# Performance work log

Hardware: AMD Instinct MI355X
Metric: run time of the kernel (lower is better)

Reference implementation:

```python
import jax, jax.numpy as jnp
import numpy as np

IN_DIM, UNITS, OUT_DIM = 128, 256, 8
DENSITY = 0.5  # 1 - sparsity_level
B, T = 256, 512


def _ncp_dims():
    Nm = OUT_DIM
    Nc = max(int(0.4 * (UNITS - Nm)), 1)   # command neurons (AutoNCP rule)
    Ni = UNITS - Nm - Nc                    # inter neurons
    return Ni, Nc, Nm


def _fanout_mask(rng, n_src, n_dst, fanout):
    # each source connects to `fanout` distinct random destinations
    idx = np.argsort(rng.random((n_src, n_dst)), axis=1)[:, :fanout]
    m = np.zeros((n_src, n_dst), dtype=np.int32)
    m[np.arange(n_src)[:, None], idx] = 1
    return m


def setup_inputs() -> dict:
    key = jax.random.key(0)
    rng = np.random.default_rng(22222)
    Ni, Nc, Nm = _ncp_dims()
    s_fan = max(int(Ni * DENSITY), 1)       # sensory fanout
    i_fan = max(int(Nc * DENSITY), 1)       # inter fanout
    m_fanin = max(int(Nc * DENSITY), 1)     # motor fanin
    M_si = _fanout_mask(rng, IN_DIM, Ni, s_fan)      # sensory -> inter
    M_ic = _fanout_mask(rng, Ni, Nc, i_fan)          # inter -> command
    M_cm = _fanout_mask(rng, Nm, Nc, m_fanin).T      # command -> motor (fanin per motor)

    def layer_mask(M_in, hid):
        # WiredCfCCell: concat input sparsity with dense ones for the recurrent block, then transpose
        return np.concatenate([M_in, np.ones((hid, hid), np.int32)], axis=0).T

    masks = [layer_mask(M_si, Ni), layer_mask(M_ic, Nc), layer_mask(M_cm, Nm)]
    dims = [(IN_DIM, Ni), (Ni, Nc), (Nc, Nm)]
    inp = {}
    for l, (fin, hid) in enumerate(dims):
        cat = fin + hid
        scale = 1.0 / np.sqrt(cat)
        for nm in ("w1", "w2", "wa", "wb"):
            inp[f"{nm}_{l}"] = jnp.asarray(rng.normal(0.0, scale, (hid, cat)).astype(np.float32))
        for nm in ("b1", "b2", "ba", "bb"):
            inp[f"{nm}_{l}"] = jnp.zeros((hid,), jnp.float32)
        inp[f"m{l}"] = jnp.asarray(masks[l])  # int32, constant sparsity mask
    k1, k2 = jax.random.split(key)
    inp["x"] = jax.random.normal(k1, (B, T, IN_DIM), jnp.float32)
    inp["dt"] = jax.random.uniform(k2, (1,), jnp.float32, 0.5, 1.5)
    return inp


def _cfc_cell(xh, w1, b1, w2, b2, wa, ba, wb, bb, m, ts):
    # CfCCell, mode='default', no backbone, sparsity mask on ff1/ff2 weights
    mf = m.astype(w1.dtype)
    ff1 = jnp.tanh(xh @ (w1 * mf).T + b1)
    ff2 = jnp.tanh(xh @ (w2 * mf).T + b2)
    t_interp = jax.nn.sigmoid((xh @ wa.T + ba) * ts + (xh @ wb.T + bb))
    return ff1 * (1.0 - t_interp) + t_interp * ff2


def _forward(x, dt, params, masks):
    Ni, Nc, Nm = _ncp_dims()
    ts = dt[0]
    h0 = jnp.zeros((x.shape[0], Ni), x.dtype)
    h1 = jnp.zeros((x.shape[0], Nc), x.dtype)
    h2 = jnp.zeros((x.shape[0], Nm), x.dtype)
    p0, p1, p2 = params

    def step(carry, xt):
        h0, h1, h2 = carry
        nh0 = _cfc_cell(jnp.concatenate([xt, h0], 1), *p0, masks[0], ts)
        nh1 = _cfc_cell(jnp.concatenate([nh0, h1], 1), *p1, masks[1], ts)
        nh2 = _cfc_cell(jnp.concatenate([nh1, h2], 1), *p2, masks[2], ts)
        return (nh0, nh1, nh2), nh2

    (h0, h1, h2), ys = jax.lax.scan(step, (h0, h1, h2), jnp.swapaxes(x, 0, 1))
    y = jnp.tanh(jnp.swapaxes(ys, 0, 1))          # (B, T, OUT_DIM), tanh output saturation
    h_out = jnp.concatenate([h0, h1, h2], axis=1)  # (B, units)
    return y, h_out


def reference(x, dt,
              w1_0, b1_0, w2_0, b2_0, wa_0, ba_0, wb_0, bb_0, m0,
              w1_1, b1_1, w2_1, b2_1, wa_1, ba_1, wb_1, bb_1, m1,
              w1_2, b1_2, w2_2, b2_2, wa_2, ba_2, wb_2, bb_2, m2):
    params = ((w1_0, b1_0, w2_0, b2_0, wa_0, ba_0, wb_0, bb_0),
              (w1_1, b1_1, w2_1, b2_1, wa_1, ba_1, wb_1, bb_1),
              (w1_2, b1_2, w2_2, b2_2, wa_2, ba_2, wb_2, bb_2))
    return _forward(x, dt, params, (m0, m1, m2))
```

## Files before the change

### kernel.cpp

```cpp
#include <hip/hip_runtime.h>
#include <cmath>


typedef _Float16 f16;
typedef f16 h4 __attribute__((ext_vector_type(4)));
typedef f16 h8 __attribute__((ext_vector_type(8)));
typedef float f4 __attribute__((ext_vector_type(4)));

#define MFMA(a, b, c) __builtin_amdgcn_mfma_f32_16x16x32_f16(a, b, c, 0, 0, 0)
#define RAW_BAR() asm volatile("s_waitcnt lgkmcnt(0)\n\ts_barrier" ::: "memory")

constexpr int IN_DIM = 128, Ni = 149, Nc = 99, Nm = 8;
constexpr int CAT0 = 277, CAT1 = 248, CAT2 = 107;
constexpr int Bsz = 256, Tsz = 512;
constexpr int TC = 128, NCH = 4, NBT = 16;
constexpr int NT0 = 30, NT1 = 21;
constexpr int S0 = 168, S2 = 136;
constexpr size_t XU0_HALVES = (size_t)TC * NBT * NT0 * 256;
constexpr size_t NH0_HALVES = (size_t)TC * NBT * 16 * 160;
constexpr size_t XU1_HALVES = (size_t)TC * NBT * NT1 * 256;
constexpr size_t H0S_HALVES = (size_t)NBT * 16 * S0;
constexpr size_t H12S_HALVES = (size_t)NBT * 2 * 16 * S2;
constexpr size_t YOFF = (size_t)Bsz * Tsz * 8;

constexpr int OFF_X0 = 0;
constexpr int OFF_R0 = 7680;
constexpr int OFF_X1 = 17280;
constexpr int OFF_R12A = 24000;
constexpr int OFF_R12B = 29376;
constexpr int NFRAG = 30144;

__device__ inline float rcpf_(float x) { return __builtin_amdgcn_rcpf(x); }
__device__ __forceinline__ float cfc_h(float a0, float a1, float a2) {
  float e0 = __expf(a0), e1 = __expf(a1), e2 = __expf(a2);
  float pa = 1.f + e0, ma = 1.f - e0;
  float pb = 1.f + e1, mb = 1.f - e1;
  float pc = 1.f + e2;
  float num = fmaf(ma * pb, e2, mb * pa);
  return num * rcpf_(pa * pb * pc);
}
__device__ __forceinline__ float tanhp_(float x) {
  float e = __expf(-2.f * x);
  return (1.f - e) * rcpf_(1.f + e);
}

__global__ __launch_bounds__(256) void pack_kernel(
    const float* __restrict__ w1_0, const float* __restrict__ w2_0,
    const float* __restrict__ wa_0, const float* __restrict__ wb_0,
    const int* __restrict__ m0,
    const float* __restrict__ w1_1, const float* __restrict__ w2_1,
    const float* __restrict__ wa_1, const float* __restrict__ wb_1,
    const int* __restrict__ m1,
    const float* __restrict__ w1_2, const float* __restrict__ w2_2,
    const float* __restrict__ wa_2, const float* __restrict__ wb_2,
    const int* __restrict__ m2, const float* __restrict__ dtp,
    f16* __restrict__ PK) {
  int idx = blockIdx.x * 256 + threadIdx.x;
  if (idx >= NFRAG) return;
  int lane = idx & 63, col = lane & 15, q = lane >> 4;
  float ts = dtp[0];
  const float* Wa = nullptr;
  const float* Wb = nullptr;
  const int* M = nullptr;
  int ld, n, nmax, k0, kmax;
  int mat;
  if (idx < OFF_R0) {
    int p = idx >> 6;
    mat = p / 40; int nt = (p >> 2) % 10, kt = p & 3;
    ld = CAT0; n = nt * 16 + col; nmax = Ni; k0 = kt * 32 + q * 8; kmax = IN_DIM;
    if (mat == 0) { Wa = w1_0; M = m0; }
    else if (mat == 1) { Wa = w2_0; M = m0; }
    else { Wa = wa_0; Wb = wb_0; }
  } else if (idx < OFF_X1) {
    int p = (idx - OFF_R0) >> 6;
    int g = p / 15; mat = (p / 5) % 3; int kt = p % 5;
    ld = CAT0; n = g * 16 + col; nmax = Ni; k0 = IN_DIM + kt * 32 + q * 8; kmax = CAT0;
    if (mat == 0) Wa = w1_0;
    else if (mat == 1) Wa = w2_0;
    else { Wa = wa_0; Wb = wb_0; }
  } else if (idx < OFF_R12A) {
    int p = (idx - OFF_X1) >> 6;
    mat = p / 35; int nt = (p / 5) % 7, kt = p % 5;
    ld = CAT1; n = nt * 16 + col; nmax = Nc; k0 = kt * 32 + q * 8; kmax = Ni;
    if (mat == 0) { Wa = w1_1; M = m1; }
    else if (mat == 1) { Wa = w2_1; M = m1; }
    else { Wa = wa_1; Wb = wb_1; }
  } else if (idx < OFF_R12B) {
    int p = (idx - OFF_R12A) >> 6;
    int wv = p / 12; mat = (p / 4) % 3; int kt = p & 3;
    ld = CAT1; n = wv * 16 + col; nmax = Nc; k0 = Ni + kt * 32 + q * 8; kmax = CAT1;
    if (mat == 0) Wa = w1_1;
    else if (mat == 1) Wa = w2_1;
    else { Wa = wa_1; Wb = wb_1; }
  } else {
    int p = (idx - OFF_R12B) >> 6;
    mat = p / 4; int kt = p & 3;
    ld = CAT2; n = col; nmax = Nm; k0 = kt * 32 + q * 8; kmax = CAT2;
    if (mat == 0) { Wa = w1_2; M = m2; }
    else if (mat == 1) { Wa = w2_2; M = m2; }
    else { Wa = wa_2; Wb = wb_2; }
  }
  h8 r;
#pragma unroll
  for (int j = 0; j < 8; j++) {
    int k = k0 + j;
    float v = 0.f;
    if (n < nmax && k < kmax) {
      if (mat < 2) {
        v = Wa[(size_t)n * ld + k];
        if (M) v *= (float)M[(size_t)n * ld + k];
        v *= -2.f;
      } else {
        v = -(ts * Wa[(size_t)n * ld + k] + Wb[(size_t)n * ld + k]);
      }
    }
    r[j] = (f16)v;
  }
  ((h8*)PK)[idx] = r;
}

__global__ __launch_bounds__(192, 2) void X_kernel(
    const h8* __restrict__ pk, const float* __restrict__ x,
    const f16* __restrict__ NH0, f16* __restrict__ XU0, f16* __restrict__ XU1,
    const float* __restrict__ b1_0, const float* __restrict__ b2_0,
    const float* __restrict__ ba_0, const float* __restrict__ bb_0,
    const float* __restrict__ b1_1, const float* __restrict__ b2_1,
    const float* __restrict__ ba_1, const float* __restrict__ bb_1,
    const float* __restrict__ dtp, int c) {
  __shared__ f16 stg[16 * 136];
  int tid = threadIdx.x;
  int w = tid >> 6, lane = tid & 63, col = lane & 15, q = lane >> 4;
  int wg = blockIdx.x;
  float ts = dtp[0];
  if (wg < 512) {
    if (c < 0) return;
    h8 Bf[7][5];
    float bias[7];
#pragma unroll
    for (int nt = 0; nt < 7; nt++) {
#pragma unroll
      for (int kt = 0; kt < 5; kt++)
        Bf[nt][kt] = pk[OFF_X1 + ((w * 7 + nt) * 5 + kt) * 64 + lane];
      int n = nt * 16 + col;
      bias[nt] = (n < Nc) ? (w == 0 ? -2.f * b1_1[n]
                                    : (w == 1 ? -2.f * b2_1[n]
                                              : -(ts * ba_1[n] + bb_1[n])))
                          : 0.f;
    }
    for (int i = 0; i < 4; i++) {
      int mt = wg * 4 + i;
      const f16* Ab = NH0 + (size_t)mt * 2560;
      h8 A[5];
#pragma unroll
      for (int kt = 0; kt < 5; kt++)
        A[kt] = *(const h8*)(Ab + col * 160 + kt * 32 + q * 8);
#pragma unroll
      for (int nt = 0; nt < 7; nt++) {
        float b = bias[nt];
        f4 acc = {b, b, b, b};
#pragma unroll
        for (int kt = 0; kt < 5; kt++) acc = MFMA(A[kt], Bf[nt][kt], acc);
        h4 o;
#pragma unroll
        for (int rr = 0; rr < 4; rr++) o[rr] = (f16)acc[rr];
        *(h4*)(XU1 + ((size_t)mt * NT1 + w * 7 + nt) * 256 + lane * 4) = o;
      }
    }
  } else {
    int cn = c + 1;
    if (cn >= NCH) return;
    int bx = wg - 512;
    h8 Bf[10][4];
    float bias[10];
#pragma unroll
    for (int nt = 0; nt < 10; nt++) {
#pragma unroll
      for (int kt = 0; kt < 4; kt++)
        Bf[nt][kt] = pk[OFF_X0 + ((w * 10 + nt) * 4 + kt) * 64 + lane];
      int n = nt * 16 + col;
      bias[nt] = (n < Ni) ? (w == 0 ? -2.f * b1_0[n]
                                    : (w == 1 ? -2.f * b2_0[n]
                                              : -(ts * ba_0[n] + bb_0[n])))
                          : 0.f;
    }
    for (int i = 0; i < 4; i++) {
      int mt = bx * 4 + i;
      int tl = mt >> 4, bt = mt & 15;
      int tg = cn * TC + tl;
      if (tid < 128) {
        int sr = tid >> 3, sc = (tid & 7) * 16;
        const float* xp = x + ((size_t)(bt * 16 + sr) * Tsz + tg) * IN_DIM + sc;
        h8 hv0, hv1;
#pragma unroll
        for (int j = 0; j < 8; j++) hv0[j] = (f16)xp[j];
#pragma unroll
        for (int j = 0; j < 8; j++) hv1[j] = (f16)xp[8 + j];
        *(h8*)(stg + sr * 136 + sc) = hv0;
        *(h8*)(stg + sr * 136 + sc + 8) = hv1;
      }
      __syncthreads();
      h8 A[4];
#pragma unroll
      for (int kt = 0; kt < 4; kt++)
        A[kt] = *(const h8*)(stg + col * 136 + kt * 32 + q * 8);
#pragma unroll
      for (int nt = 0; nt < 10; nt++) {
        float b = bias[nt];
        f4 acc = {b, b, b, b};
#pragma unroll
        for (int kt = 0; kt < 4; kt++) acc = MFMA(A[kt], Bf[nt][kt], acc);
        h4 o;
#pragma unroll
        for (int rr = 0; rr < 4; rr++) o[rr] = (f16)acc[rr];
        *(h4*)(XU0 + ((size_t)mt * NT0 + w * 10 + nt) * 256 + lane * 4) = o;
      }
      __syncthreads();
    }
  }
}

__device__ __forceinline__ void r0_step(
    const f16* br, f16* bw, const f16* __restrict__ XU0, f16* __restrict__ NH0,
    float* __restrict__ out, const h8 (&Bf)[3][5], h4 (&xu)[3],
    int t, int tload, int bt, int g, int lane, int col, int q, int n, bool last) {
  h8 A[5];
#pragma unroll
  for (int kt = 0; kt < 5; kt++)
    A[kt] = *(const h8*)(br + col * S0 + kt * 32 + q * 8);
  f4 acc0 = {(float)xu[0][0], (float)xu[0][1], (float)xu[0][2], (float)xu[0][3]};
  f4 acc1 = {(float)xu[1][0], (float)xu[1][1], (float)xu[1][2], (float)xu[1][3]};
  f4 acc2 = {(float)xu[2][0], (float)xu[2][1], (float)xu[2][2], (float)xu[2][3]};
  size_t mtl = (size_t)tload * NBT + bt;
#pragma unroll
  for (int mat = 0; mat < 3; mat++)
    xu[mat] = *(const h4*)(XU0 + (mtl * NT0 + mat * 10 + g) * 256 + lane * 4);
#pragma unroll
  for (int kt = 0; kt < 5; kt++) {
    acc0 = MFMA(A[kt], Bf[0][kt], acc0);
    acc1 = MFMA(A[kt], Bf[1][kt], acc1);
    acc2 = MFMA(A[kt], Bf[2][kt], acc2);
  }
  int mt = t * NBT + bt;
  f16* nh = NH0 + (size_t)mt * 2560;
#pragma unroll
  for (int r = 0; r < 4; r++) {
    int m = q * 4 + r;
    float h = cfc_h(acc0[r], acc1[r], acc2[r]);
    f16 h16 = (f16)h;
    bw[m * S0 + n] = h16;
    nh[m * 160 + n] = h16;
    if (last && n < Ni) out[YOFF + (size_t)(bt * 16 + m) * 256 + n] = h;
  }
}

__device__ __forceinline__ void r12l1_step(
    const f16* br, f16* bw, const f16* __restrict__ XU1, float* __restrict__ out,
    const h8 (&Bf)[3][4], h4 (&xu)[3],
    int tload, int bt, int w, int lane, int col, int q, int n, bool last) {
  h8 A[4];
#pragma unroll
  for (int kt = 0; kt < 4; kt++)
    A[kt] = *(const h8*)(br + col * S2 + kt * 32 + q * 8);
  f4 acc0 = {(float)xu[0][0], (float)xu[0][1], (float)xu[0][2], (float)xu[0][3]};
  f4 acc1 = {(float)xu[1][0], (float)xu[1][1], (float)xu[1][2], (float)xu[1][3]};
  f4 acc2 = {(float)xu[2][0], (float)xu[2][1], (float)xu[2][2], (float)xu[2][3]};
  size_t mtl = (size_t)tload * NBT + bt;
#pragma unroll
  for (int mat = 0; mat < 3; mat++)
    xu[mat] = *(const h4*)(XU1 + (mtl * NT1 + mat * 7 + w) * 256 + lane * 4);
#pragma unroll
  for (int kt = 0; kt < 4; kt++) {
    acc0 = MFMA(A[kt], Bf[0][kt], acc0);
    acc1 = MFMA(A[kt], Bf[1][kt], acc1);
    acc2 = MFMA(A[kt], Bf[2][kt], acc2);
  }
#pragma unroll
  for (int r = 0; r < 4; r++) {
    int m = q * 4 + r;
    float h = cfc_h(acc0[r], acc1[r], acc2[r]);
    if (n < Nc) {
      bw[m * S2 + n] = (f16)h;
      if (last) out[YOFF + (size_t)(bt * 16 + m) * 256 + Ni + n] = h;
    }
  }
}

__device__ __forceinline__ void r12l2_step(
    const f16* rb, f16* wb, float* __restrict__ out, const h8 (&Bf)[3][4],
    float bn0, float bn1, float bn2, int tg, int bt, int col, int q, bool last) {
  h8 A[4];
#pragma unroll
  for (int kt = 0; kt < 4; kt++)
    A[kt] = *(const h8*)(rb + col * S2 + kt * 32 + q * 8);
  f4 acc0 = {bn0, bn0, bn0, bn0};
  f4 acc1 = {bn1, bn1, bn1, bn1};
  f4 acc2 = {bn2, bn2, bn2, bn2};
#pragma unroll
  for (int kt = 0; kt < 4; kt++) {
    acc0 = MFMA(A[kt], Bf[0][kt], acc0);
    acc1 = MFMA(A[kt], Bf[1][kt], acc1);
    acc2 = MFMA(A[kt], Bf[2][kt], acc2);
  }
#pragma unroll
  for (int r = 0; r < 4; r++) {
    int m = q * 4 + r;
    float h = cfc_h(acc0[r], acc1[r], acc2[r]);
    if (col < Nm) {
      out[((size_t)(bt * 16 + m) * Tsz + tg) * 8 + col] = tanhp_(h);
      wb[m * S2 + Nc + col] = (f16)h;
      if (last) out[YOFF + (size_t)(bt * 16 + m) * 256 + Ni + Nc + col] = h;
    }
  }
}

__global__ __launch_bounds__(640) void R_kernel(
    const h8* __restrict__ pk,
    const float* __restrict__ c1, const float* __restrict__ c2,
    const float* __restrict__ ca, const float* __restrict__ cb,
    const float* __restrict__ dtp, const f16* __restrict__ XU0,
    const f16* __restrict__ XU1, f16* __restrict__ NH0,
    f16* __restrict__ H0S, f16* __restrict__ H12S, float* __restrict__ out, int c) {
  __shared__ __align__(16) char smem[2 * 16 * S0 * 2];
  int tid = threadIdx.x;
  int g = tid >> 6, lane = tid & 63, col = lane & 15, q = lane >> 4;
  int wg = blockIdx.x;

  if (wg < NBT) {
    if (c >= NCH) return;
    f16(*buf)[16 * S0] = (f16(*)[16 * S0])smem;
    int bt = wg;
    int n = g * 16 + col;
    h8 Bf[3][5];
#pragma unroll
    for (int mat = 0; mat < 3; mat++)
#pragma unroll
      for (int kt = 0; kt < 5; kt++)
        Bf[mat][kt] = pk[OFF_R0 + ((g * 3 + mat) * 5 + kt) * 64 + lane];

    for (int idx = tid; idx < 16 * S0; idx += 640) {
      buf[0][idx] = (c == 0) ? (f16)0.f : H0S[(size_t)bt * 16 * S0 + idx];
      buf[1][idx] = (f16)0.f;
    }
    __syncthreads();

    h4 xuA[3], xuB[3];
#pragma unroll
    for (int mat = 0; mat < 3; mat++) {
      xuA[mat] = *(const h4*)(XU0 + ((size_t)bt * NT0 + mat * 10 + g) * 256 + lane * 4);
      xuB[mat] =
          *(const h4*)(XU0 + ((size_t)(NBT + bt) * NT0 + mat * 10 + g) * 256 + lane * 4);
    }

    for (int t = 0; t < TC; t += 2) {
      bool lastA = (c == NCH - 1) && (t == TC - 1);
      int tlA = (t + 2 < TC) ? t + 2 : t;
      r0_step(buf[0], buf[1], XU0, NH0, out, Bf, xuA, t, tlA, bt, g, lane, col, q, n,
              lastA);
      RAW_BAR();
      bool lastB = (c == NCH - 1) && (t + 1 == TC - 1);
      int tlB = (t + 3 < TC) ? t + 3 : t + 1;
      r0_step(buf[1], buf[0], XU0, NH0, out, Bf, xuB, t + 1, tlB, bt, g, lane, col, q,
              n, lastB);
      RAW_BAR();
    }
    for (int idx = tid; idx < 16 * S0; idx += 640)
      H0S[(size_t)bt * 16 * S0 + idx] = buf[0][idx];

  } else {
    int cc = c - 1;
    if (cc < 0) return;
    f16(*buf)[16 * S2] = (f16(*)[16 * S2])smem;
    int bt = wg - NBT;
    int w = g;
    float ts = dtp[0];
    h8 Bf[3][4];
    float bn0 = 0.f, bn1 = 0.f, bn2 = 0.f;
    int n = w * 16 + col;
    if (w < 7) {
#pragma unroll
      for (int mat = 0; mat < 3; mat++)
#pragma unroll
        for (int kt = 0; kt < 4; kt++)
          Bf[mat][kt] = pk[OFF_R12A + ((w * 3 + mat) * 4 + kt) * 64 + lane];
    } else if (w == 7) {
#pragma unroll
      for (int mat = 0; mat < 3; mat++)
#pragma unroll
        for (int kt = 0; kt < 4; kt++)
          Bf[mat][kt] = pk[OFF_R12B + (mat * 4 + kt) * 64 + lane];
      bn0 = (col < Nm) ? -2.f * c1[col] : 0.f;
      bn1 = (col < Nm) ? -2.f * c2[col] : 0.f;
      bn2 = (col < Nm) ? -(ts * ca[col] + cb[col]) : 0.f;
    }
    for (int idx = tid; idx < 2 * 16 * S2; idx += 640)
      ((f16*)buf)[idx] = (cc == 0) ? (f16)0.f : H12S[(size_t)bt * 2 * 16 * S2 + idx];
    __syncthreads();

    h4 xuA[3], xuB[3];
    if (w < 7) {
#pragma unroll
      for (int mat = 0; mat < 3; mat++) {
        xuA[mat] =
            *(const h4*)(XU1 + ((size_t)bt * NT1 + mat * 7 + w) * 256 + lane * 4);
        xuB[mat] = *(const h4*)(XU1 +
                                ((size_t)(NBT + bt) * NT1 + mat * 7 + w) * 256 +
                                lane * 4);
      }
    }

    for (int t = 0; t < TC; t += 2) {
      if (w < 7) {
        int tlA = (t + 2 < TC) ? t + 2 : t;
        bool lastA = (cc == NCH - 1) && (t == TC - 1);
        r12l1_step(buf[0], buf[1], XU1, out, Bf, xuA, tlA, bt, w, lane, col, q, n,
                   lastA);
      }
      RAW_BAR();
      if (w == 7)
        r12l2_step(buf[1], buf[0], out, Bf, bn0, bn1, bn2, cc * TC + t, bt, col, q,
                   false);
      if (w < 7) {
        int tlB = (t + 3 < TC) ? t + 3 : t + 1;
        bool lastB = (cc == NCH - 1) && (t + 1 == TC - 1);
        r12l1_step(buf[1], buf[0], XU1, out, Bf, xuB, tlB, bt, w, lane, col, q, n,
                   lastB);
      }
      RAW_BAR();
      if (w == 7)
        r12l2_step(buf[0], buf[1], out, Bf, bn0, bn1, bn2, cc * TC + t + 1, bt, col, q,
                   (cc == NCH - 1) && (t + 1 == TC - 1));
    }
    __syncthreads();
    for (int idx = tid; idx < 2 * 16 * S2; idx += 640)
      H12S[(size_t)bt * 2 * 16 * S2 + idx] = ((f16*)buf)[idx];
  }
}

extern "C" void kernel_launch(void* const* d_in, const int* in_sizes, int n_in,
                              void* d_out, int out_size, void* d_ws, size_t ws_size,
                              hipStream_t stream) {
  const float* w1_0 = (const float*)d_in[0];
  const float* w2_0 = (const float*)d_in[1];
  const float* wa_0 = (const float*)d_in[2];
  const float* wb_0 = (const float*)d_in[3];
  const float* b1_0 = (const float*)d_in[4];
  const float* b2_0 = (const float*)d_in[5];
  const float* ba_0 = (const float*)d_in[6];
  const float* bb_0 = (const float*)d_in[7];
  const int* m0 = (const int*)d_in[8];
  const float* w1_1 = (const float*)d_in[9];
  const float* w2_1 = (const float*)d_in[10];
  const float* wa_1 = (const float*)d_in[11];
  const float* wb_1 = (const float*)d_in[12];
  const float* b1_1 = (const float*)d_in[13];
  const float* b2_1 = (const float*)d_in[14];
  const float* ba_1 = (const float*)d_in[15];
  const float* bb_1 = (const float*)d_in[16];
  const int* m1 = (const int*)d_in[17];
  const float* w1_2 = (const float*)d_in[18];
  const float* w2_2 = (const float*)d_in[19];
  const float* wa_2 = (const float*)d_in[20];
  const float* wb_2 = (const float*)d_in[21];
  const float* c1 = (const float*)d_in[22];
  const float* c2 = (const float*)d_in[23];
  const float* ca = (const float*)d_in[24];
  const float* cb = (const float*)d_in[25];
  const int* m2 = (const int*)d_in[26];
  const float* x = (const float*)d_in[27];
  const float* dt = (const float*)d_in[28];
  float* out = (float*)d_out;

  f16* XU0 = (f16*)d_ws;
  f16* NH0 = XU0 + XU0_HALVES;
  f16* XU1 = NH0 + NH0_HALVES;
  f16* H0S = XU1 + XU1_HALVES;
  f16* H12S = H0S + H0S_HALVES;
  f16* PK = H12S + H12S_HALVES;
  const h8* pk = (const h8*)PK;

  pack_kernel<<<(NFRAG + 255) / 256, 256, 0, stream>>>(
      w1_0, w2_0, wa_0, wb_0, m0, w1_1, w2_1, wa_1, wb_1, m1,
      w1_2, w2_2, wa_2, wb_2, m2, dt, PK);

  X_kernel<<<1024, 192, 0, stream>>>(pk, x, NH0, XU0, XU1, b1_0, b2_0, ba_0, bb_0,
                                     b1_1, b2_1, ba_1, bb_1, dt, -1);

  for (int c = 0; c <= NCH; c++) {
    R_kernel<<<32, 640, 0, stream>>>(pk, c1, c2, ca, cb, dt, XU0, XU1, NH0, H0S,
                                     H12S, out, c);
    if (c < NCH)
      X_kernel<<<1024, 192, 0, stream>>>(pk, x, NH0, XU0, XU1, b1_0, b2_0, ba_0,
                                         bb_0, b1_1, b2_1, ba_1, bb_1, dt, c);
  }
}
```

Before: 826.9 us.

## Fuse X projections into recurrent kernel with double-buffered chunk pipeline

Merges the separate input-projection kernel into the recurrent kernel. Extra workgroups compute the next chunk's layer-0 input projection while the recurrent workgroups run the current chunk. The layer-1 input projection is now computed inline by the layer-0 recurrent waves right after each hidden state is produced, so the NH0 round trip through global memory is gone. XU buffers are double-buffered across chunks, the chunk size is halved so the stages overlap more, and the projection tiles are packed densely to drop the padding tiles. The trade-off is extra MFMA work on the latency-critical recurrent path and more launches of one larger kernel.

```diff
diff --git a/kernel.cpp b/kernel.cpp
--- a/kernel.cpp
+++ b/kernel.cpp
@@ -13,22 +13,24 @@
 constexpr int IN_DIM = 128, Ni = 149, Nc = 99, Nm = 8;
 constexpr int CAT0 = 277, CAT1 = 248, CAT2 = 107;
 constexpr int Bsz = 256, Tsz = 512;
-constexpr int TC = 128, NCH = 4, NBT = 16;
-constexpr int NT0 = 30, NT1 = 21;
+constexpr int TC = 64, NCH = 8, NBT = 16;
+constexpr int NT0P = 28;
+constexpr int NT1P = 19;
 constexpr int S0 = 168, S2 = 136;
-constexpr size_t XU0_HALVES = (size_t)TC * NBT * NT0 * 256;
-constexpr size_t NH0_HALVES = (size_t)TC * NBT * 16 * 160;
-constexpr size_t XU1_HALVES = (size_t)TC * NBT * NT1 * 256;
-constexpr size_t H0S_HALVES = (size_t)NBT * 16 * S0;
-constexpr size_t H12S_HALVES = (size_t)NBT * 2 * 16 * S2;
+constexpr size_t XU0_H = (size_t)TC * NBT * NT0P * 256;
+constexpr size_t XU1_H = (size_t)TC * NBT * NT1P * 256;
+constexpr size_t H0S_H = (size_t)NBT * 16 * S0;
+constexpr size_t H12S_H = (size_t)NBT * 2 * 16 * S2;
 constexpr size_t YOFF = (size_t)Bsz * Tsz * 8;
+constexpr size_t XUST0 = (size_t)NBT * NT0P * 256;
+constexpr size_t XUST1 = (size_t)NBT * NT1P * 256;
 
 constexpr int OFF_X0 = 0;
-constexpr int OFF_R0 = 7680;
-constexpr int OFF_X1 = 17280;
-constexpr int OFF_R12A = 24000;
-constexpr int OFF_R12B = 29376;
-constexpr int NFRAG = 30144;
+constexpr int OFF_R0 = 7168;
+constexpr int OFF_X1 = 16768;
+constexpr int OFF_R12A = 22848;
+constexpr int OFF_R12B = 28224;
+constexpr int NFRAG = 28992;
 
 __device__ inline float rcpf_(float x) { return __builtin_amdgcn_rcpf(x); }
 __device__ __forceinline__ float cfc_h(float a0, float a1, float a2) {
@@ -42,6 +44,15 @@
 __device__ __forceinline__ float tanhp_(float x) {
   float e = __expf(-2.f * x);
   return (1.f - e) * rcpf_(1.f + e);
+}
+__device__ __forceinline__ float xbias(int j, int period, int maxj,
+                                       const float* b1, const float* b2,
+                                       const float* ba, const float* bb, float ts) {
+  if (j >= maxj) return 0.f;
+  int mat = j / period, nn = j - mat * period;
+  if (mat == 0) return -2.f * b1[nn];
+  if (mat == 1) return -2.f * b2[nn];
+  return -(ts * ba[nn] + bb[nn]);
 }
 
 __global__ __launch_bounds__(256) void pack_kernel(
@@ -59,284 +70,229 @@
   if (idx >= NFRAG) return;
   int lane = idx & 63, col = lane & 15, q = lane >> 4;
   float ts = dtp[0];
-  const float* Wa = nullptr;
-  const float* Wb = nullptr;
+  const float* W1;  const float* W2;  const float* Wa;  const float* Wb;
   const int* M = nullptr;
-  int ld, n, nmax, k0, kmax;
-  int mat;
+  int ld, n = 0, mat = 0, k0 = 0, kmax = 0;
+  bool valid = true;
   if (idx < OFF_R0) {
     int p = idx >> 6;
-    mat = p / 40; int nt = (p >> 2) % 10, kt = p & 3;
-    ld = CAT0; n = nt * 16 + col; nmax = Ni; k0 = kt * 32 + q * 8; kmax = IN_DIM;
-    if (mat == 0) { Wa = w1_0; M = m0; }
-    else if (mat == 1) { Wa = w2_0; M = m0; }
-    else { Wa = wa_0; Wb = wb_0; }
+    int ti = p >> 2, kt = p & 3;
+    int j = ti * 16 + col;
+    W1 = w1_0; W2 = w2_0; Wa = wa_0; Wb = wb_0;
+    ld = CAT0; kmax = IN_DIM; k0 = kt * 32 + q * 8;
+    if (j < 447) { mat = j / 149; n = j - mat * 149; if (mat < 2) M = m0; }
+    else valid = false;
   } else if (idx < OFF_X1) {
     int p = (idx - OFF_R0) >> 6;
     int g = p / 15; mat = (p / 5) % 3; int kt = p % 5;
-    ld = CAT0; n = g * 16 + col; nmax = Ni; k0 = IN_DIM + kt * 32 + q * 8; kmax = CAT0;
-    if (mat == 0) Wa = w1_0;
-    else if (mat == 1) Wa = w2_0;
-    else { Wa = wa_0; Wb = wb_0; }
+    W1 = w1_0; W2 = w2_0; Wa = wa_0; Wb = wb_0;
+    ld = CAT0; kmax = CAT0; k0 = IN_DIM + kt * 32 + q * 8;
+    n = g * 16 + col;
+    if (n >= Ni) valid = false;
   } else if (idx < OFF_R12A) {
     int p = (idx - OFF_X1) >> 6;
-    mat = p / 35; int nt = (p / 5) % 7, kt = p % 5;
-    ld = CAT1; n = nt * 16 + col; nmax = Nc; k0 = kt * 32 + q * 8; kmax = Ni;
-    if (mat == 0) { Wa = w1_1; M = m1; }
-    else if (mat == 1) { Wa = w2_1; M = m1; }
-    else { Wa = wa_1; Wb = wb_1; }
+    int ti = p / 5, kt = p % 5;
+    int j = ti * 16 + col;
+    W1 = w1_1; W2 = w2_1; Wa = wa_1; Wb = wb_1;
+    ld = CAT1; kmax = Ni; k0 = kt * 32 + q * 8;
+    if (j < 297) { mat = j / 99; n = j - mat * 99; if (mat < 2) M = m1; }
+    else valid = false;
   } else if (idx < OFF_R12B) {
     int p = (idx - OFF_R12A) >> 6;
-    int wv = p / 12; mat = (p / 4) % 3; int kt = p & 3;
-    ld = CAT1; n = wv * 16 + col; nmax = Nc; k0 = Ni + kt * 32 + q * 8; kmax = CAT1;
-    if (mat == 0) Wa = w1_1;
-    else if (mat == 1) Wa = w2_1;
-    else { Wa = wa_1; Wb = wb_1; }
+    int w = p / 12; mat = (p / 4) % 3; int kt = p & 3;
+    W1 = w1_1; W2 = w2_1; Wa = wa_1; Wb = wb_1;
+    ld = CAT1; kmax = CAT1; k0 = Ni + kt * 32 + q * 8;
+    n = w * 16 + col;
+    if (n >= Nc) valid = false;
   } else {
     int p = (idx - OFF_R12B) >> 6;
     mat = p / 4; int kt = p & 3;
-    ld = CAT2; n = col; nmax = Nm; k0 = kt * 32 + q * 8; kmax = CAT2;
-    if (mat == 0) { Wa = w1_2; M = m2; }
-    else if (mat == 1) { Wa = w2_2; M = m2; }
-    else { Wa = wa_2; Wb = wb_2; }
+    W1 = w1_2; W2 = w2_2; Wa = wa_2; Wb = wb_2;
+    ld = CAT2; kmax = CAT2; k0 = kt * 32 + q * 8;
+    n = col;
+    if (n >= Nm) valid = false;
+    else if (mat < 2) M = m2;
   }
   h8 r;
 #pragma unroll
   for (int j = 0; j < 8; j++) {
     int k = k0 + j;
     float v = 0.f;
-    if (n < nmax && k < kmax) {
-      if (mat < 2) {
-        v = Wa[(size_t)n * ld + k];
-        if (M) v *= (float)M[(size_t)n * ld + k];
-        v *= -2.f;
-      } else {
-        v = -(ts * Wa[(size_t)n * ld + k] + Wb[(size_t)n * ld + k]);
-      }
+    if (valid && k < kmax) {
+      if (mat == 0) v = -2.f * W1[(size_t)n * ld + k];
+      else if (mat == 1) v = -2.f * W2[(size_t)n * ld + k];
+      else v = -(ts * Wa[(size_t)n * ld + k] + Wb[(size_t)n * ld + k]);
+      if (M) v *= (float)M[(size_t)n * ld + k];
     }
     r[j] = (f16)v;
   }
   ((h8*)PK)[idx] = r;
 }
 
-__global__ __launch_bounds__(192, 2) void X_kernel(
+__device__ __forceinline__ void r0_step(
+    const f16* br, f16* bw, const f16* const (&xub)[3], int tload,
+    const h8 (&Bf)[3][5], h4 (&xu)[3],
+    const h8 (&Bfx)[2][5], const float (&bx)[2], f16* const (&stx)[2],
+    int tstore, bool do_x1, bool skip2,
+    float* __restrict__ out, int bt, int q, int col, int n, bool last) {
+  h8 A[5];
+#pragma unroll
+  for (int kt = 0; kt < 5; kt++)
+    A[kt] = *(const h8*)(br + col * S0 + kt * 32 + q * 8);
+  f4 a0 = {(float)xu[0][0], (float)xu[0][1], (float)xu[0][2], (float)xu[0][3]};
+  f4 a1 = {(float)xu[1][0], (float)xu[1][1], (float)xu[1][2], (float)xu[1][3]};
+  f4 a2 = {(float)xu[2][0], (float)xu[2][1], (float)xu[2][2], (float)xu[2][3]};
+#pragma unroll
+  for (int mat = 0; mat < 3; mat++)
+    xu[mat] = *(const h4*)(xub[mat] + (size_t)tload * XUST0);
+#pragma unroll
+  for (int kt = 0; kt < 5; kt++) {
+    a0 = MFMA(A[kt], Bf[0][kt], a0);
+    a1 = MFMA(A[kt], Bf[1][kt], a1);
+    a2 = MFMA(A[kt], Bf[2][kt], a2);
+  }
+  if (do_x1) {
+#pragma unroll
+    for (int tt = 0; tt < 2; tt++) {
+      float b = bx[tt];
+      f4 ax = {b, b, b, b};
+#pragma unroll
+      for (int kt = 0; kt < 5; kt++) ax = MFMA(A[kt], Bfx[tt][kt], ax);
+      h4 o;
+#pragma unroll
+      for (int rr = 0; rr < 4; rr++) o[rr] = (f16)ax[rr];
+      if (!(skip2 && tt == 1))
+        *(h4*)(stx[tt] + (size_t)tstore * XUST1) = o;
+    }
+  }
+#pragma unroll
+  for (int r = 0; r < 4; r++) {
+    int m = q * 4 + r;
+    float h = cfc_h(a0[r], a1[r], a2[r]);
+    f16 h16 = (f16)h;
+    bw[m * S0 + n] = h16;
+    if (last && n < Ni) out[YOFF + (size_t)(bt * 16 + m) * 256 + n] = h;
+  }
+}
+
+__device__ __forceinline__ void r12l1_step(
+    const f16* br, f16* bw, const f16* const (&xub)[3], int tload,
+    const h8 (&Bf)[3][4], h4 (&xu)[3],
+    float* __restrict__ out, int bt, int q, int col, int n, bool last) {
+  h8 A[4];
+#pragma unroll
+  for (int kt = 0; kt < 4; kt++)
+    A[kt] = *(const h8*)(br + col * S2 + kt * 32 + q * 8);
+  f4 a0 = {(float)xu[0][0], (float)xu[0][1], (float)xu[0][2], (float)xu[0][3]};
+  f4 a1 = {(float)xu[1][0], (float)xu[1][1], (float)xu[1][2], (float)xu[1][3]};
+  f4 a2 = {(float)xu[2][0], (float)xu[2][1], (float)xu[2][2], (float)xu[2][3]};
+#pragma unroll
+  for (int mat = 0; mat < 3; mat++)
+    xu[mat] = *(const h4*)(xub[mat] + (size_t)tload * XUST1);
+#pragma unroll
+  for (int kt = 0; kt < 4; kt++) {
+    a0 = MFMA(A[kt], Bf[0][kt], a0);
+    a1 = MFMA(A[kt], Bf[1][kt], a1);
+    a2 = MFMA(A[kt], Bf[2][kt], a2);
+  }
+#pragma unroll
+  for (int r = 0; r < 4; r++) {
+    int m = q * 4 + r;
+    float h = cfc_h(a0[r], a1[r], a2[r]);
+    if (n < Nc) {
+      bw[m * S2 + n] = (f16)h;
+      if (last) out[YOFF + (size_t)(bt * 16 + m) * 256 + Ni + n] = h;
+    }
+  }
+}
+
+__device__ __forceinline__ void r12l2_step(
+    const f16* rb, f16* wb, float* __restrict__ out, const h8 (&Bf)[3][4],
+    float bn0, float bn1, float bn2, int tg, int bt, int col, int q, bool last) {
+  h8 A[4];
+#pragma unroll
+  for (int kt = 0; kt < 4; kt++)
+    A[kt] = *(const h8*)(rb + col * S2 + kt * 32 + q * 8);
+  f4 a0 = {bn0, bn0, bn0, bn0};
+  f4 a1 = {bn1, bn1, bn1, bn1};
+  f4 a2 = {bn2, bn2, bn2, bn2};
+#pragma unroll
+  for (int kt = 0; kt < 4; kt++) {
+    a0 = MFMA(A[kt], Bf[0][kt], a0);
+    a1 = MFMA(A[kt], Bf[1][kt], a1);
+    a2 = MFMA(A[kt], Bf[2][kt], a2);
+  }
+#pragma unroll
+  for (int r = 0; r < 4; r++) {
+    int m = q * 4 + r;
+    float h = cfc_h(a0[r], a1[r], a2[r]);
+    if (col < Nm) {
+      out[((size_t)(bt * 16 + m) * Tsz + tg) * 8 + col] = tanhp_(h);
+      wb[m * S2 + Nc + col] = (f16)h;
+      if (last) out[YOFF + (size_t)(bt * 16 + m) * 256 + Ni + Nc + col] = h;
+    }
+  }
+}
+
+__global__ __launch_bounds__(640, 3) void R_kernel(
     const h8* __restrict__ pk, const float* __restrict__ x,
-    const f16* __restrict__ NH0, f16* __restrict__ XU0, f16* __restrict__ XU1,
     const float* __restrict__ b1_0, const float* __restrict__ b2_0,
     const float* __restrict__ ba_0, const float* __restrict__ bb_0,
     const float* __restrict__ b1_1, const float* __restrict__ b2_1,
     const float* __restrict__ ba_1, const float* __restrict__ bb_1,
-    const float* __restrict__ dtp, int c) {
-  __shared__ f16 stg[16 * 136];
-  int tid = threadIdx.x;
-  int w = tid >> 6, lane = tid & 63, col = lane & 15, q = lane >> 4;
-  int wg = blockIdx.x;
-  float ts = dtp[0];
-  if (wg < 512) {
-    if (c < 0) return;
-    h8 Bf[7][5];
-    float bias[7];
-#pragma unroll
-    for (int nt = 0; nt < 7; nt++) {
-#pragma unroll
-      for (int kt = 0; kt < 5; kt++)
-        Bf[nt][kt] = pk[OFF_X1 + ((w * 7 + nt) * 5 + kt) * 64 + lane];
-      int n = nt * 16 + col;
-      bias[nt] = (n < Nc) ? (w == 0 ? -2.f * b1_1[n]
-                                    : (w == 1 ? -2.f * b2_1[n]
-                                              : -(ts * ba_1[n] + bb_1[n])))
-                          : 0.f;
-    }
-    for (int i = 0; i < 4; i++) {
-      int mt = wg * 4 + i;
-      const f16* Ab = NH0 + (size_t)mt * 2560;
-      h8 A[5];
-#pragma unroll
-      for (int kt = 0; kt < 5; kt++)
-        A[kt] = *(const h8*)(Ab + col * 160 + kt * 32 + q * 8);
-#pragma unroll
-      for (int nt = 0; nt < 7; nt++) {
-        float b = bias[nt];
-        f4 acc = {b, b, b, b};
-#pragma unroll
-        for (int kt = 0; kt < 5; kt++) acc = MFMA(A[kt], Bf[nt][kt], acc);
-        h4 o;
-#pragma unroll
-        for (int rr = 0; rr < 4; rr++) o[rr] = (f16)acc[rr];
-        *(h4*)(XU1 + ((size_t)mt * NT1 + w * 7 + nt) * 256 + lane * 4) = o;
-      }
-    }
-  } else {
-    int cn = c + 1;
-    if (cn >= NCH) return;
-    int bx = wg - 512;
-    h8 Bf[10][4];
-    float bias[10];
-#pragma unroll
-    for (int nt = 0; nt < 10; nt++) {
-#pragma unroll
-      for (int kt = 0; kt < 4; kt++)
-        Bf[nt][kt] = pk[OFF_X0 + ((w * 10 + nt) * 4 + kt) * 64 + lane];
-      int n = nt * 16 + col;
-      bias[nt] = (n < Ni) ? (w == 0 ? -2.f * b1_0[n]
-                                    : (w == 1 ? -2.f * b2_0[n]
-                                              : -(ts * ba_0[n] + bb_0[n])))
-                          : 0.f;
-    }
-    for (int i = 0; i < 4; i++) {
-      int mt = bx * 4 + i;
-      int tl = mt >> 4, bt = mt & 15;
-      int tg = cn * TC + tl;
-      if (tid < 128) {
-        int sr = tid >> 3, sc = (tid & 7) * 16;
-        const float* xp = x + ((size_t)(bt * 16 + sr) * Tsz + tg) * IN_DIM + sc;
-        h8 hv0, hv1;
-#pragma unroll
-        for (int j = 0; j < 8; j++) hv0[j] = (f16)xp[j];
-#pragma unroll
-        for (int j = 0; j < 8; j++) hv1[j] = (f16)xp[8 + j];
-        *(h8*)(stg + sr * 136 + sc) = hv0;
-        *(h8*)(stg + sr * 136 + sc + 8) = hv1;
-      }
-      __syncthreads();
-      h8 A[4];
-#pragma unroll
-      for (int kt = 0; kt < 4; kt++)
-        A[kt] = *(const h8*)(stg + col * 136 + kt * 32 + q * 8);
-#pragma unroll
-      for (int nt = 0; nt < 10; nt++) {
-        float b = bias[nt];
-        f4 acc = {b, b, b, b};
-#pragma unroll
-        for (int kt = 0; kt < 4; kt++) acc = MFMA(A[kt], Bf[nt][kt], acc);
-        h4 o;
-#pragma unroll
-        for (int rr = 0; rr < 4; rr++) o[rr] = (f16)acc[rr];
-        *(h4*)(XU0 + ((size_t)mt * NT0 + w * 10 + nt) * 256 + lane * 4) = o;
-      }
-      __syncthreads();
-    }
-  }
-}
-
-__device__ __forceinline__ void r0_step(
-    const f16* br, f16* bw, const f16* __restrict__ XU0, f16* __restrict__ NH0,
-    float* __restrict__ out, const h8 (&Bf)[3][5], h4 (&xu)[3],
-    int t, int tload, int bt, int g, int lane, int col, int q, int n, bool last) {
-  h8 A[5];
-#pragma unroll
-  for (int kt = 0; kt < 5; kt++)
-    A[kt] = *(const h8*)(br + col * S0 + kt * 32 + q * 8);
-  f4 acc0 = {(float)xu[0][0], (float)xu[0][1], (float)xu[0][2], (float)xu[0][3]};
-  f4 acc1 = {(float)xu[1][0], (float)xu[1][1], (float)xu[1][2], (float)xu[1][3]};
-  f4 acc2 = {(float)xu[2][0], (float)xu[2][1], (float)xu[2][2], (float)xu[2][3]};
-  size_t mtl = (size_t)tload * NBT + bt;
-#pragma unroll
-  for (int mat = 0; mat < 3; mat++)
-    xu[mat] = *(const h4*)(XU0 + (mtl * NT0 + mat * 10 + g) * 256 + lane * 4);
-#pragma unroll
-  for (int kt = 0; kt < 5; kt++) {
-    acc0 = MFMA(A[kt], Bf[0][kt], acc0);
-    acc1 = MFMA(A[kt], Bf[1][kt], acc1);
-    acc2 = MFMA(A[kt], Bf[2][kt], acc2);
-  }
-  int mt = t * NBT + bt;
-  f16* nh = NH0 + (size_t)mt * 2560;
-#pragma unroll
-  for (int r = 0; r < 4; r++) {
-    int m = q * 4 + r;
-    float h = cfc_h(acc0[r], acc1[r], acc2[r]);
-    f16 h16 = (f16)h;
-    bw[m * S0 + n] = h16;
-    nh[m * 160 + n] = h16;
-    if (last && n < Ni) out[YOFF + (size_t)(bt * 16 + m) * 256 + n] = h;
-  }
-}
-
-__device__ __forceinline__ void r12l1_step(
-    const f16* br, f16* bw, const f16* __restrict__ XU1, float* __restrict__ out,
-    const h8 (&Bf)[3][4], h4 (&xu)[3],
-    int tload, int bt, int w, int lane, int col, int q, int n, bool last) {
-  h8 A[4];
-#pragma unroll
-  for (int kt = 0; kt < 4; kt++)
-    A[kt] = *(const h8*)(br + col * S2 + kt * 32 + q * 8);
-  f4 acc0 = {(float)xu[0][0], (float)xu[0][1], (float)xu[0][2], (float)xu[0][3]};
-  f4 acc1 = {(float)xu[1][0], (float)xu[1][1], (float)xu[1][2], (float)xu[1][3]};
-  f4 acc2 = {(float)xu[2][0], (float)xu[2][1], (float)xu[2][2], (float)xu[2][3]};
-  size_t mtl = (size_t)tload * NBT + bt;
-#pragma unroll
-  for (int mat = 0; mat < 3; mat++)
-    xu[mat] = *(const h4*)(XU1 + (mtl * NT1 + mat * 7 + w) * 256 + lane * 4);
-#pragma unroll
-  for (int kt = 0; kt < 4; kt++) {
-    acc0 = MFMA(A[kt], Bf[0][kt], acc0);
-    acc1 = MFMA(A[kt], Bf[1][kt], acc1);
-    acc2 = MFMA(A[kt], Bf[2][kt], acc2);
-  }
-#pragma unroll
-  for (int r = 0; r < 4; r++) {
-    int m = q * 4 + r;
-    float h = cfc_h(acc0[r], acc1[r], acc2[r]);
-    if (n < Nc) {
-      bw[m * S2 + n] = (f16)h;
-      if (last) out[YOFF + (size_t)(bt * 16 + m) * 256 + Ni + n] = h;
-    }
-  }
-}
-
-__device__ __forceinline__ void r12l2_step(
-    const f16* rb, f16* wb, float* __restrict__ out, const h8 (&Bf)[3][4],
-    float bn0, float bn1, float bn2, int tg, int bt, int col, int q, bool last) {
-  h8 A[4];
-#pragma unroll
-  for (int kt = 0; kt < 4; kt++)
-    A[kt] = *(const h8*)(rb + col * S2 + kt * 32 + q * 8);
-  f4 acc0 = {bn0, bn0, bn0, bn0};
-  f4 acc1 = {bn1, bn1, bn1, bn1};
-  f4 acc2 = {bn2, bn2, bn2, bn2};
-#pragma unroll
-  for (int kt = 0; kt < 4; kt++) {
-    acc0 = MFMA(A[kt], Bf[0][kt], acc0);
-    acc1 = MFMA(A[kt], Bf[1][kt], acc1);
-    acc2 = MFMA(A[kt], Bf[2][kt], acc2);
-  }
-#pragma unroll
-  for (int r = 0; r < 4; r++) {
-    int m = q * 4 + r;
-    float h = cfc_h(acc0[r], acc1[r], acc2[r]);
-    if (col < Nm) {
-      out[((size_t)(bt * 16 + m) * Tsz + tg) * 8 + col] = tanhp_(h);
-      wb[m * S2 + Nc + col] = (f16)h;
-      if (last) out[YOFF + (size_t)(bt * 16 + m) * 256 + Ni + Nc + col] = h;
-    }
-  }
-}
-
-__global__ __launch_bounds__(640) void R_kernel(
-    const h8* __restrict__ pk,
     const float* __restrict__ c1, const float* __restrict__ c2,
     const float* __restrict__ ca, const float* __restrict__ cb,
-    const float* __restrict__ dtp, const f16* __restrict__ XU0,
-    const f16* __restrict__ XU1, f16* __restrict__ NH0,
-    f16* __restrict__ H0S, f16* __restrict__ H12S, float* __restrict__ out, int c) {
+    const float* __restrict__ dtp,
+    f16* __restrict__ XU0a, f16* __restrict__ XU0b,
+    f16* __restrict__ XU1a, f16* __restrict__ XU1b,
+    f16* __restrict__ H0S, f16* __restrict__ H12S,
+    float* __restrict__ out, int c) {
   __shared__ __align__(16) char smem[2 * 16 * S0 * 2];
   int tid = threadIdx.x;
   int g = tid >> 6, lane = tid & 63, col = lane & 15, q = lane >> 4;
   int wg = blockIdx.x;
+  float ts = dtp[0];
 
   if (wg < NBT) {
-    if (c >= NCH) return;
+    if (c < 0 || c >= NCH) return;
     f16(*buf)[16 * S0] = (f16(*)[16 * S0])smem;
     int bt = wg;
     int n = g * 16 + col;
+    const f16* XU0r = (c & 1) ? XU0b : XU0a;
+    f16* XU1w = (c & 1) ? XU1b : XU1a;
     h8 Bf[3][5];
 #pragma unroll
     for (int mat = 0; mat < 3; mat++)
 #pragma unroll
       for (int kt = 0; kt < 5; kt++)
         Bf[mat][kt] = pk[OFF_R0 + ((g * 3 + mat) * 5 + kt) * 64 + lane];
-
+    bool skip2 = (g == 9);
+    int ti0 = skip2 ? 18 : 2 * g;
+    int ti1 = skip2 ? 18 : 2 * g + 1;
+    h8 Bfx[2][5];
+    float bx[2];
+    f16* stx[2];
+    {
+      int tis[2] = {ti0, ti1};
+#pragma unroll
+      for (int tt = 0; tt < 2; tt++) {
+#pragma unroll
+        for (int kt = 0; kt < 5; kt++)
+          Bfx[tt][kt] = pk[OFF_X1 + (tis[tt] * 5 + kt) * 64 + lane];
+        bx[tt] = xbias(tis[tt] * 16 + col, 99, 297, b1_1, b2_1, ba_1, bb_1, ts);
+        stx[tt] = XU1w + ((size_t)bt * NT1P + tis[tt]) * 256 + lane * 4;
+      }
+    }
+    const f16* xub[3];
+    {
+      int nn = n < 148 ? n : 148;
+#pragma unroll
+      for (int mat = 0; mat < 3; mat++) {
+        int cm = mat * 149 + nn;
+        xub[mat] = XU0r + ((size_t)bt * NT0P + (cm >> 4)) * 256 +
+                   (q * 16 + (cm & 15)) * 4;
+      }
+    }
     for (int idx = tid; idx < 16 * S0; idx += 640) {
       buf[0][idx] = (c == 0) ? (f16)0.f : H0S[(size_t)bt * 16 * S0 + idx];
       buf[1][idx] = (f16)0.f;
@@ -346,42 +302,66 @@
     h4 xuA[3], xuB[3];
 #pragma unroll
     for (int mat = 0; mat < 3; mat++) {
-      xuA[mat] = *(const h4*)(XU0 + ((size_t)bt * NT0 + mat * 10 + g) * 256 + lane * 4);
-      xuB[mat] =
-          *(const h4*)(XU0 + ((size_t)(NBT + bt) * NT0 + mat * 10 + g) * 256 + lane * 4);
+      xuA[mat] = *(const h4*)(xub[mat]);
+      xuB[mat] = *(const h4*)(xub[mat] + XUST1 * 0 + XUST0);
     }
 
     for (int t = 0; t < TC; t += 2) {
-      bool lastA = (c == NCH - 1) && (t == TC - 1);
-      int tlA = (t + 2 < TC) ? t + 2 : t;
-      r0_step(buf[0], buf[1], XU0, NH0, out, Bf, xuA, t, tlA, bt, g, lane, col, q, n,
-              lastA);
+      int tlA = (t + 2 < TC) ? t + 2 : TC - 1;
+      r0_step(buf[0], buf[1], xub, tlA, Bf, xuA, Bfx, bx, stx, t - 1, t > 0, skip2,
+              out, bt, q, col, n, false);
       RAW_BAR();
+      int tlB = (t + 3 < TC) ? t + 3 : TC - 1;
       bool lastB = (c == NCH - 1) && (t + 1 == TC - 1);
-      int tlB = (t + 3 < TC) ? t + 3 : t + 1;
-      r0_step(buf[1], buf[0], XU0, NH0, out, Bf, xuB, t + 1, tlB, bt, g, lane, col, q,
-              n, lastB);
+      r0_step(buf[1], buf[0], xub, tlB, Bf, xuB, Bfx, bx, stx, t, true, skip2,
+              out, bt, q, col, n, lastB);
       RAW_BAR();
+    }
+    {
+      h8 A[5];
+#pragma unroll
+      for (int kt = 0; kt < 5; kt++)
+        A[kt] = *(const h8*)(buf[0] + col * S0 + kt * 32 + q * 8);
+#pragma unroll
+      for (int tt = 0; tt < 2; tt++) {
+        float b = bx[tt];
+        f4 ax = {b, b, b, b};
+#pragma unroll
+        for (int kt = 0; kt < 5; kt++) ax = MFMA(A[kt], Bfx[tt][kt], ax);
+        h4 o;
+#pragma unroll
+        for (int rr = 0; rr < 4; rr++) o[rr] = (f16)ax[rr];
+        if (!(skip2 && tt == 1))
+          *(h4*)(stx[tt] + (size_t)(TC - 1) * XUST1) = o;
+      }
     }
     for (int idx = tid; idx < 16 * S0; idx += 640)
       H0S[(size_t)bt * 16 * S0 + idx] = buf[0][idx];
 
-  } else {
+  } else if (wg < 2 * NBT) {
     int cc = c - 1;
-    if (cc < 0) return;
+    if (cc < 0 || cc >= NCH) return;
     f16(*buf)[16 * S2] = (f16(*)[16 * S2])smem;
     int bt = wg - NBT;
     int w = g;
-    float ts = dtp[0];
+    const f16* XU1r = (cc & 1) ? XU1b : XU1a;
     h8 Bf[3][4];
     float bn0 = 0.f, bn1 = 0.f, bn2 = 0.f;
     int n = w * 16 + col;
+    const f16* xub[3] = {XU1r, XU1r, XU1r};
     if (w < 7) {
 #pragma unroll
       for (int mat = 0; mat < 3; mat++)
 #pragma unroll
         for (int kt = 0; kt < 4; kt++)
           Bf[mat][kt] = pk[OFF_R12A + ((w * 3 + mat) * 4 + kt) * 64 + lane];
+      int nn = n < 98 ? n : 98;
+#pragma unroll
+      for (int mat = 0; mat < 3; mat++) {
+        int cm = mat * 99 + nn;
+        xub[mat] = XU1r + ((size_t)bt * NT1P + (cm >> 4)) * 256 +
+                   (q * 16 + (cm & 15)) * 4;
+      }
     } else if (w == 7) {
 #pragma unroll
       for (int mat = 0; mat < 3; mat++)
@@ -400,39 +380,84 @@
     if (w < 7) {
 #pragma unroll
       for (int mat = 0; mat < 3; mat++) {
-        xuA[mat] =
-            *(const h4*)(XU1 + ((size_t)bt * NT1 + mat * 7 + w) * 256 + lane * 4);
-        xuB[mat] = *(const h4*)(XU1 +
-                                ((size_t)(NBT + bt) * NT1 + mat * 7 + w) * 256 +
-                                lane * 4);
-      }
-    }
-
+        xuA[mat] = *(const h4*)(xub[mat]);
+        xuB[mat] = *(const h4*)(xub[mat] + XUST1);
+      }
+    }
     for (int t = 0; t < TC; t += 2) {
       if (w < 7) {
-        int tlA = (t + 2 < TC) ? t + 2 : t;
-        bool lastA = (cc == NCH - 1) && (t == TC - 1);
-        r12l1_step(buf[0], buf[1], XU1, out, Bf, xuA, tlA, bt, w, lane, col, q, n,
-                   lastA);
+        int tlA = (t + 2 < TC) ? t + 2 : TC - 1;
+        r12l1_step(buf[0], buf[1], xub, tlA, Bf, xuA, out, bt, q, col, n, false);
       }
       RAW_BAR();
       if (w == 7)
         r12l2_step(buf[1], buf[0], out, Bf, bn0, bn1, bn2, cc * TC + t, bt, col, q,
                    false);
       if (w < 7) {
-        int tlB = (t + 3 < TC) ? t + 3 : t + 1;
+        int tlB = (t + 3 < TC) ? t + 3 : TC - 1;
         bool lastB = (cc == NCH - 1) && (t + 1 == TC - 1);
-        r12l1_step(buf[1], buf[0], XU1, out, Bf, xuB, tlB, bt, w, lane, col, q, n,
-                   lastB);
+        r12l1_step(buf[1], buf[0], xub, tlB, Bf, xuB, out, bt, q, col, n, lastB);
       }
       RAW_BAR();
       if (w == 7)
-        r12l2_step(buf[0], buf[1], out, Bf, bn0, bn1, bn2, cc * TC + t + 1, bt, col, q,
-                   (cc == NCH - 1) && (t + 1 == TC - 1));
+        r12l2_step(buf[0], buf[1], out, Bf, bn0, bn1, bn2, cc * TC + t + 1, bt, col,
+                   q, (cc == NCH - 1) && (t + 1 == TC - 1));
     }
     __syncthreads();
     for (int idx = tid; idx < 2 * 16 * S2; idx += 640)
       H12S[(size_t)bt * 2 * 16 * S2 + idx] = ((f16*)buf)[idx];
+
+  } else {
+    int cn = c + 1;
+    if (cn >= NCH) return;
+    f16* stg = (f16*)smem;
+    f16* XU0w = (cn & 1) ? XU0b : XU0a;
+    int wgx = wg - 2 * NBT;
+    bool w9 = (g == 9);
+    h8 Bfx0[3][4];
+    float bx0[3];
+    int tis[3];
+#pragma unroll
+    for (int tt = 0; tt < 3; tt++) {
+      int ti = 3 * g + tt;
+      if (ti > 27) ti = 27;
+      tis[tt] = ti;
+#pragma unroll
+      for (int kt = 0; kt < 4; kt++)
+        Bfx0[tt][kt] = pk[OFF_X0 + (ti * 4 + kt) * 64 + lane];
+      bx0[tt] = xbias(ti * 16 + col, 149, 447, b1_0, b2_0, ba_0, bb_0, ts);
+    }
+    for (int i = 0; i < 8; i++) {
+      int mt = wgx * 8 + i;
+      int tl = mt >> 4, bt = mt & 15;
+      int tg = cn * TC + tl;
+      if (tid < 256) {
+        int sr = tid >> 4, scv = (tid & 15) * 8;
+        const float* xp = x + ((size_t)(bt * 16 + sr) * Tsz + tg) * IN_DIM + scv;
+        h8 hv;
+#pragma unroll
+        for (int j = 0; j < 8; j++) hv[j] = (f16)xp[j];
+        *(h8*)(stg + sr * 136 + scv) = hv;
+      }
+      __syncthreads();
+      h8 A[4];
+#pragma unroll
+      for (int kt = 0; kt < 4; kt++)
+        A[kt] = *(const h8*)(stg + col * 136 + kt * 32 + q * 8);
+#pragma unroll
+      for (int tt = 0; tt < 3; tt++) {
+        float b = bx0[tt];
+        f4 ax = {b, b, b, b};
+#pragma unroll
+        for (int kt = 0; kt < 4; kt++) ax = MFMA(A[kt], Bfx0[tt][kt], ax);
+        h4 o;
+#pragma unroll
+        for (int rr = 0; rr < 4; rr++) o[rr] = (f16)ax[rr];
+        if (!(w9 && tt > 0))
+          *(h4*)(XU0w + ((size_t)mt * NT0P + tis[tt]) * 256 + lane * 4) = o;
+      }
+      __syncthreads();
+    }
   }
 }
 
@@ -470,26 +495,22 @@
   const float* dt = (const float*)d_in[28];
   float* out = (float*)d_out;
 
-  f16* XU0 = (f16*)d_ws;
-  f16* NH0 = XU0 + XU0_HALVES;
-  f16* XU1 = NH0 + NH0_HALVES;
-  f16* H0S = XU1 + XU1_HALVES;
-  f16* H12S = H0S + H0S_HALVES;
-  f16* PK = H12S + H12S_HALVES;
+  f16* XU0a = (f16*)d_ws;
+  f16* XU0b = XU0a + XU0_H;
+  f16* XU1a = XU0b + XU0_H;
+  f16* XU1b = XU1a + XU1_H;
+  f16* H0S = XU1b + XU1_H;
+  f16* H12S = H0S + H0S_H;
+  f16* PK = H12S + H12S_H;
   const h8* pk = (const h8*)PK;
 
   pack_kernel<<<(NFRAG + 255) / 256, 256, 0, stream>>>(
       w1_0, w2_0, wa_0, wb_0, m0, w1_1, w2_1, wa_1, wb_1, m1,
       w1_2, w2_2, wa_2, wb_2, m2, dt, PK);
 
-  X_kernel<<<1024, 192, 0, stream>>>(pk, x, NH0, XU0, XU1, b1_0, b2_0, ba_0, bb_0,
-                                     b1_1, b2_1, ba_1, bb_1, dt, -1);
-
-  for (int c = 0; c <= NCH; c++) {
-    R_kernel<<<32, 640, 0, stream>>>(pk, c1, c2, ca, cb, dt, XU0, XU1, NH0, H0S,
-                                     H12S, out, c);
-    if (c < NCH)
-      X_kernel<<<1024, 192, 0, stream>>>(pk, x, NH0, XU0, XU1, b1_0, b2_0, ba_0,
-                                         bb_0, b1_1, b2_1, ba_1, bb_1, dt, c);
-  }
-}
+  for (int c = -1; c <= NCH; c++) {
+    R_kernel<<<160, 640, 0, stream>>>(pk, x, b1_0, b2_0, ba_0, bb_0, b1_1, b2_1,
+                                      ba_1, bb_1, c1, c2, ca, cb, dt, XU0a, XU0b,
+                                      XU1a, XU1b, H0S, H12S, out, c);
+  }
+}
```

Result: slower. 1.414 ms (+71.1%).
